# Kernel optimization log

Hardware: AMD Instinct MI355X
Metric: run time of the kernel (lower is better)

The kernel has to match this reference:

```python
import jax, jax.numpy as jnp
import numpy as np

N_HEADS = 8  # from init_kwargs; only used for the softmax scale


def setup_inputs() -> dict:
    key = jax.random.key(0)
    k1, k2, k3 = jax.random.split(key, 3)
    B, S, D = 4, 4096, 1024
    inputs = jax.random.normal(k1, (B, S, 2 * D), dtype=jnp.float32)
    W_qkv = jax.random.normal(k2, (2 * D, 3 * D), dtype=jnp.float32) * (1.0 / np.sqrt(2 * D))
    W_ff = jax.random.normal(k3, (D, D), dtype=jnp.float32) * (1.0 / np.sqrt(D))
    b_ff = jnp.zeros((D,), dtype=jnp.float32)
    return {"inputs": inputs, "W_qkv": W_qkv, "W_ff": W_ff, "b_ff": b_ff}


def reference(inputs, W_qkv, W_ff, b_ff):
    D = W_ff.shape[0]
    dim_head = D / N_HEADS
    scale = 1.0 / np.sqrt(dim_head)
    kqv = inputs @ W_qkv                       # [B, S, 3D]
    k, q, v = jnp.split(kqv, 3, axis=-1)        # chunk order in source: k, q, v
    scores = jnp.einsum('bqd,bkd->bqk', q, k) * scale   # [B, S, S]
    attn = jax.nn.softmax(scores, axis=-1)
    # dropout_p is undefined in the buggy source; treated as eval-mode identity
    out = jnp.einsum('bqk,bkd->bqd', attn, v)   # [B, S, D]
    return out @ W_ff + b_ff
```

## Files before the change

### kernel.cpp

```cpp
#include <hip/hip_runtime.h>

typedef unsigned short u16;
using bf16x8 = __attribute__((ext_vector_type(8))) __bf16;
using f32x4  = __attribute__((ext_vector_type(4))) float;
using u16x8  = __attribute__((ext_vector_type(8))) u16;

__device__ __forceinline__ u16 f2bf(float f) {
    unsigned u = __builtin_bit_cast(unsigned, f);
    u += 0x7FFFu + ((u >> 16) & 1u);
    return (u16)(u >> 16);
}
__device__ __forceinline__ float bf2f(u16 h) {
    unsigned u = ((unsigned)h) << 16;
    return __builtin_bit_cast(float, u);
}
__device__ __forceinline__ u16 to_bf(float f) { return f2bf(f); }
__device__ __forceinline__ u16 to_bf(u16 h)   { return h; }

__device__ __forceinline__ void gload_lds16(const u16* g, u16* l) {
    __builtin_amdgcn_global_load_lds(
        (const __attribute__((address_space(1))) unsigned int*)g,
        (__attribute__((address_space(3))) unsigned int*)l,
        16, 0, 0);
}

__global__ __launch_bounds__(256) void k_cvt_f32_bf16(const float* __restrict__ in,
                                                      u16* __restrict__ out, long n) {
    long i = ((long)blockIdx.x * 256 + threadIdx.x) * 8;
    if (i + 8 > n) return;
    f32x4 a = *(const f32x4*)(in + i);
    f32x4 b = *(const f32x4*)(in + i + 4);
    u16x8 o;
    o[0] = f2bf(a[0]); o[1] = f2bf(a[1]); o[2] = f2bf(a[2]); o[3] = f2bf(a[3]);
    o[4] = f2bf(b[0]); o[5] = f2bf(b[1]); o[6] = f2bf(b[2]); o[7] = f2bf(b[3]);
    *(u16x8*)(out + i) = o;
}

template <typename T>
__global__ __launch_bounds__(256) void k_transpose_bf16(
    const T* __restrict__ in, long in_rs, long in_bs,
    u16* __restrict__ out, long out_rs, long out_bs, int R, int C) {
    __shared__ u16 tile[32][33];
    const int b = blockIdx.z;
    const T* ip = in + (long)b * in_bs;
    u16* op = out + (long)b * out_bs;
    const int tx = threadIdx.x, ty = threadIdx.y;
    const long r0 = (long)blockIdx.y * 32, c0 = (long)blockIdx.x * 32;
#pragma unroll
    for (int i = 0; i < 4; ++i) {
        int r = ty + i * 8;
        tile[r][tx] = to_bf(ip[(r0 + r) * in_rs + c0 + tx]);
    }
    __syncthreads();
#pragma unroll
    for (int i = 0; i < 4; ++i) {
        int c = ty + i * 8;
        op[(c0 + c) * out_rs + r0 + tx] = tile[tx][c];
    }
}

__global__ __launch_bounds__(256) void k_rowsum_recip(const u16* __restrict__ P,
                                                      float* __restrict__ out, int C) {
    const long row = blockIdx.x;
    const u16* p = P + row * (long)C;
    float s = 0.f;
    for (int c = threadIdx.x * 8; c < C; c += 256 * 8) {
        u16x8 v = *(const u16x8*)(p + c);
#pragma unroll
        for (int j = 0; j < 8; ++j) s += bf2f(v[j]);
    }
#pragma unroll
    for (int off = 32; off > 0; off >>= 1) s += __shfl_down(s, off);
    __shared__ float wsum[4];
    const int lane = threadIdx.x & 63, wid = threadIdx.x >> 6;
    if (lane == 0) wsum[wid] = s;
    __syncthreads();
    if (threadIdx.x == 0) out[row] = 1.0f / (wsum[0] + wsum[1] + wsum[2] + wsum[3]);
}


#define LGK0 asm volatile("s_waitcnt lgkmcnt(0)" ::: "memory")
#define VM4  asm volatile("s_waitcnt vmcnt(4)" ::: "memory")
#define VM0  asm volatile("s_waitcnt vmcnt(0)" ::: "memory")
#define SCHB __builtin_amdgcn_sched_barrier(0)
#define BAR  __builtin_amdgcn_s_barrier()

template <int EPI>
__global__ __launch_bounds__(512, 2) void k_gemm8(
    const u16* __restrict__ Ag, long lda, long sA,
    const u16* __restrict__ Bg, long ldb, long sB,
    void* __restrict__ Cv, long ldc, long sC,
    int K, float scale, const float* __restrict__ rrowZ, long sR,
    const float* __restrict__ bias) {
    __shared__ __align__(16) u16 As[2][2][256 * 32];
    __shared__ __align__(16) u16 Bs[2][2][256 * 32];

    const int tid = threadIdx.x;
    const int lane = tid & 63, wid = tid >> 6;
    const int wm = wid >> 2, wn = wid & 3;
    const int z = blockIdx.z;
    const long m0 = (long)blockIdx.y * 256;
    const long n0 = (long)blockIdx.x * 256;
    const u16* A = Ag + (long)z * sA;
    const u16* B = Bg + (long)z * sB;

    int st_idx[2]; long aRow[2], bRow[2];
#pragma unroll
    for (int c = 0; c < 2; ++c) {
        int d_lin = (wid * 2 + c) * 1024 + lane * 16;
        int d_log = d_lin ^ (((d_lin >> 9) & 1) << 5);
        int r = d_log >> 6, kk = (d_log & 63) >> 1;
        st_idx[c] = (wid * 2 + c) * 512;
        aRow[c] = (m0 + r) * lda + kk;
        bRow[c] = (n0 + r) * ldb + kk;
    }
    const int aBase = (wm * 128 + (lane & 15)) * 64 + (lane >> 4) * 16;
    const int bBase = (wn * 64 + (lane & 15)) * 64 + (lane >> 4) * 16;

#define STG_A(pb, ks, kt) do { \
        gload_lds16(A + aRow[0] + (kt) + (ks) * 32, &As[pb][ks][st_idx[0]]); \
        gload_lds16(A + aRow[1] + (kt) + (ks) * 32, &As[pb][ks][st_idx[1]]); } while (0)
#define STG_B(pb, ks, kt) do { \
        gload_lds16(B + bRow[0] + (kt) + (ks) * 32, &Bs[pb][ks][st_idx[0]]); \
        gload_lds16(B + bRow[1] + (kt) + (ks) * 32, &Bs[pb][ks][st_idx[1]]); } while (0)
#define LD_A(dst, mf, ks, pb) do { int _o = aBase + (mf) * 1024; \
        _o ^= ((_o >> 9) & 1) << 5; \
        (dst) = *(const bf16x8*)((const char*)&As[pb][ks][0] + _o); } while (0)
#define LD_B(dst, nf, ks, pb) do { int _o = bBase + (nf) * 1024; \
        _o ^= ((_o >> 9) & 1) << 5; \
        (dst) = *(const bf16x8*)((const char*)&Bs[pb][ks][0] + _o); } while (0)
#define MM16(mb) do { \
        _Pragma("unroll") for (int mf = 0; mf < 4; ++mf) \
        _Pragma("unroll") for (int nf = 0; nf < 4; ++nf) \
            acc[(mb) + mf][nf] = __builtin_amdgcn_mfma_f32_16x16x32_bf16( \
                afr[mf], bfr[nf], acc[(mb) + mf][nf], 0, 0, 0); } while (0)

#define KTILE(pb, STG, ktn) do { \
         \
        _Pragma("unroll") for (int i = 0; i < 4; ++i) LD_A(afr[i], i, 0, pb); \
        _Pragma("unroll") for (int i = 0; i < 4; ++i) LD_B(bfr[i], i, 0, pb); \
        if (STG) STG_A((pb) ^ 1, 0, ktn); \
        BAR; LGK0; SCHB; \
        __builtin_amdgcn_s_setprio(1); MM16(0); __builtin_amdgcn_s_setprio(0); \
        BAR; \
         \
        _Pragma("unroll") for (int i = 0; i < 4; ++i) LD_A(afr[i], 4 + i, 0, pb); \
        if (STG) STG_B((pb) ^ 1, 0, ktn); \
        BAR; LGK0; SCHB; \
        __builtin_amdgcn_s_setprio(1); MM16(4); __builtin_amdgcn_s_setprio(0); \
        if (STG) { VM4; } else { VM0; } \
        BAR; SCHB; \
         \
        _Pragma("unroll") for (int i = 0; i < 4; ++i) LD_A(afr[i], i, 1, pb); \
        _Pragma("unroll") for (int i = 0; i < 4; ++i) LD_B(bfr[i], i, 1, pb); \
        if (STG) STG_A((pb) ^ 1, 1, ktn); \
        BAR; LGK0; SCHB; \
        __builtin_amdgcn_s_setprio(1); MM16(0); __builtin_amdgcn_s_setprio(0); \
        BAR; \
         \
        _Pragma("unroll") for (int i = 0; i < 4; ++i) LD_A(afr[i], 4 + i, 1, pb); \
        if (STG) STG_B((pb) ^ 1, 1, ktn); \
        BAR; LGK0; SCHB; \
        __builtin_amdgcn_s_setprio(1); MM16(4); __builtin_amdgcn_s_setprio(0); \
        if (STG) { VM4; } \
        BAR; SCHB; \
    } while (0)

    f32x4 acc[8][4] = {};
    bf16x8 afr[4], bfr[4];

    STG_A(0, 0, 0); STG_B(0, 0, 0); STG_A(0, 1, 0); STG_B(0, 1, 0);
    VM4;
    BAR; SCHB;

    const int NT = K >> 6;
    int p = 0;
    for (int t = 0; t < NT - 1; ++t) {
        KTILE(p, 1, (t + 1) * 64);
        p ^= 1;
    }
    KTILE(p, 0, 0);

    const int r_in = (lane >> 4) * 4;
    const int c_in = lane & 15;
    const float* rr = (EPI == 2) ? (rrowZ + (long)z * sR) : nullptr;
#pragma unroll
    for (int mf = 0; mf < 8; ++mf) {
#pragma unroll
        for (int nf = 0; nf < 4; ++nf) {
            const long cg = n0 + wn * 64 + nf * 16 + c_in;
#pragma unroll
            for (int j = 0; j < 4; ++j) {
                const long rg = m0 + wm * 128 + mf * 16 + r_in + j;
                float v = acc[mf][nf][j];
                if constexpr (EPI == 0) {
                    ((u16*)Cv)[(long)z * sC + rg * ldc + cg] = f2bf(v);
                } else if constexpr (EPI == 1) {
                    ((u16*)Cv)[(long)z * sC + rg * ldc + cg] = f2bf(__expf(v * scale));
                } else if constexpr (EPI == 2) {
                    ((u16*)Cv)[(long)z * sC + rg * ldc + cg] = f2bf(v * rr[rg]);
                } else {
                    ((float*)Cv)[(long)z * sC + rg * ldc + cg] = v + bias[cg];
                }
            }
        }
    }
#undef KTILE
#undef MM16
#undef LD_A
#undef LD_B
#undef STG_A
#undef STG_B
}

extern "C" void kernel_launch(void* const* d_in, const int* in_sizes, int n_in,
                              void* d_out, int out_size, void* d_ws, size_t ws_size,
                              hipStream_t stream) {
    (void)in_sizes; (void)n_in; (void)out_size;
    const int S = 4096;
    const long BS = 4L * S;
    const float* x_f    = (const float*)d_in[0];
    const float* Wqkv_f = (const float*)d_in[1];
    const float* Wff_f  = (const float*)d_in[2];
    const float* bff    = (const float*)d_in[3];
    float* out = (float*)d_out;

    const size_t need4 = 67108864UL + 12582912UL + 2097152UL + 100663296UL +
                         33554432UL + 4UL * 33554432UL + 33554432UL + 65536UL;
    const bool batched = ws_size >= need4;
    const int Z = batched ? 4 : 1;

    char* p = (char*)d_ws;
    u16* x_bf  = (u16*)p; p += BS * 2048 * 2;
    u16* WqkvT = (u16*)p; p += 3072L * 2048 * 2;
    u16* WffT  = (u16*)p; p += 1024L * 1024 * 2;
    u16* kqv   = (u16*)p; p += BS * 3072 * 2;
    u16* vT    = (u16*)p; p += 4L * 1024 * 4096 * 2;
    u16* probs = (u16*)p; p += (long)Z * 4096L * 4096 * 2;
    u16* attn  = (u16*)p; p += BS * 1024 * 2;
    float* rrow = (float*)p; p += (long)Z * 4096L * 4;

    k_cvt_f32_bf16<<<dim3((unsigned)(BS * 2048 / 2048)), 256, 0, stream>>>(x_f, x_bf, BS * 2048);
    k_transpose_bf16<float><<<dim3(3072 / 32, 2048 / 32, 1), dim3(32, 8), 0, stream>>>(
        Wqkv_f, 3072, 0, WqkvT, 2048, 0, 2048, 3072);
    k_transpose_bf16<float><<<dim3(1024 / 32, 1024 / 32, 1), dim3(32, 8), 0, stream>>>(
        Wff_f, 1024, 0, WffT, 1024, 0, 1024, 1024);

    k_gemm8<0><<<dim3(3072 / 256, 16384 / 256, 1), 512, 0, stream>>>(
        x_bf, 2048, 0, WqkvT, 2048, 0, kqv, 3072, 0, 2048, 0.f, nullptr, 0, nullptr);

    k_transpose_bf16<u16><<<dim3(1024 / 32, 4096 / 32, 4), dim3(32, 8), 0, stream>>>(
        kqv + 2048, 3072, (long)S * 3072, vT, 4096, 1024L * 4096, 4096, 1024);

    const float scale = 0.08838834764831845f;
    for (int b = 0; b < 4; b += Z) {
        const u16* kbase = kqv + (long)b * S * 3072;
        k_gemm8<1><<<dim3(4096 / 256, 4096 / 256, Z), 512, 0, stream>>>(
            kbase + 1024, 3072, (long)S * 3072, kbase, 3072, (long)S * 3072,
            probs, 4096, (long)S * S, 1024, scale, nullptr, 0, nullptr);
        k_rowsum_recip<<<Z * 4096, 256, 0, stream>>>(probs, rrow, 4096);
        k_gemm8<2><<<dim3(1024 / 256, 4096 / 256, Z), 512, 0, stream>>>(
            probs, 4096, (long)S * S, vT + (long)b * 1024 * 4096, 4096, 1024L * 4096,
            attn + (long)b * S * 1024, 1024, (long)S * 1024,
            4096, 0.f, rrow, 4096, nullptr);
    }

    k_gemm8<3><<<dim3(1024 / 256, 16384 / 256, 1), 512, 0, stream>>>(
        attn, 1024, 0, WffT, 1024, 0, out, 1024, 0, 1024, 0.f, nullptr, 0, bff);
}
```

Baseline: 742.0 us.

## Double-buffer MFMA register fragments to overlap LDS reads with matrix math

Replaces the single set of A/B register fragments with two ping-pong sets in the GEMM main loop. The LDS reads for the next MFMA block are issued before the current block's MFMAs, and partial lgkmcnt waits (4/8) replace full waits. The goal is to hide LDS read latency behind MFMA execution. It raises register pressure under the 512-thread, 2-block launch bound, and the hand-tuned wait counts and barriers have to stay exactly right for correctness.

After: 745.3 us. About the same (+0.4%).

```diff
diff --git a/kernel.cpp b/kernel.cpp
--- a/kernel.cpp
+++ b/kernel.cpp
@@ -79,11 +79,12 @@
 }
 
 
-#define LGK0 asm volatile("s_waitcnt lgkmcnt(0)" ::: "memory")
-#define VM4  asm volatile("s_waitcnt vmcnt(4)" ::: "memory")
-#define VM0  asm volatile("s_waitcnt vmcnt(0)" ::: "memory")
-#define SCHB __builtin_amdgcn_sched_barrier(0)
-#define BAR  __builtin_amdgcn_s_barrier()
+#define LGK(n) asm volatile("s_waitcnt lgkmcnt(" #n ")" ::: "memory")
+#define VMC(n) asm volatile("s_waitcnt vmcnt(" #n ")" ::: "memory")
+#define SCHB   __builtin_amdgcn_sched_barrier(0)
+#define BAR    __builtin_amdgcn_s_barrier()
+#define PRIO1  __builtin_amdgcn_s_setprio(1)
+#define PRIO0  __builtin_amdgcn_s_setprio(0)
 
 template <int EPI>
 __global__ __launch_bounds__(512, 2) void k_gemm8(
@@ -123,63 +124,79 @@
 #define STG_B(pb, ks, kt) do { \
         gload_lds16(B + bRow[0] + (kt) + (ks) * 32, &Bs[pb][ks][st_idx[0]]); \
         gload_lds16(B + bRow[1] + (kt) + (ks) * 32, &Bs[pb][ks][st_idx[1]]); } while (0)
-#define LD_A(dst, mf, ks, pb) do { int _o = aBase + (mf) * 1024; \
-        _o ^= ((_o >> 9) & 1) << 5; \
-        (dst) = *(const bf16x8*)((const char*)&As[pb][ks][0] + _o); } while (0)
-#define LD_B(dst, nf, ks, pb) do { int _o = bBase + (nf) * 1024; \
-        _o ^= ((_o >> 9) & 1) << 5; \
-        (dst) = *(const bf16x8*)((const char*)&Bs[pb][ks][0] + _o); } while (0)
-#define MM16(mb) do { \
+#define LD4_A(dst, h, ks, pb) do { \
+        _Pragma("unroll") for (int _i = 0; _i < 4; ++_i) { \
+            int _o = aBase + ((h) * 4 + _i) * 1024; \
+            _o ^= ((_o >> 9) & 1) << 5; \
+            dst[_i] = *(const bf16x8*)((const char*)&As[pb][ks][0] + _o); } } while (0)
+#define LD4_B(dst, ks, pb) do { \
+        _Pragma("unroll") for (int _i = 0; _i < 4; ++_i) { \
+            int _o = bBase + _i * 1024; \
+            _o ^= ((_o >> 9) & 1) << 5; \
+            dst[_i] = *(const bf16x8*)((const char*)&Bs[pb][ks][0] + _o); } } while (0)
+#define MM16(mb, af, bf) do { \
         _Pragma("unroll") for (int mf = 0; mf < 4; ++mf) \
         _Pragma("unroll") for (int nf = 0; nf < 4; ++nf) \
             acc[(mb) + mf][nf] = __builtin_amdgcn_mfma_f32_16x16x32_bf16( \
-                afr[mf], bfr[nf], acc[(mb) + mf][nf], 0, 0, 0); } while (0)
-
-#define KTILE(pb, STG, ktn) do { \
-         \
-        _Pragma("unroll") for (int i = 0; i < 4; ++i) LD_A(afr[i], i, 0, pb); \
-        _Pragma("unroll") for (int i = 0; i < 4; ++i) LD_B(bfr[i], i, 0, pb); \
-        if (STG) STG_A((pb) ^ 1, 0, ktn); \
-        BAR; LGK0; SCHB; \
-        __builtin_amdgcn_s_setprio(1); MM16(0); __builtin_amdgcn_s_setprio(0); \
-        BAR; \
-         \
-        _Pragma("unroll") for (int i = 0; i < 4; ++i) LD_A(afr[i], 4 + i, 0, pb); \
-        if (STG) STG_B((pb) ^ 1, 0, ktn); \
-        BAR; LGK0; SCHB; \
-        __builtin_amdgcn_s_setprio(1); MM16(4); __builtin_amdgcn_s_setprio(0); \
-        if (STG) { VM4; } else { VM0; } \
-        BAR; SCHB; \
-         \
-        _Pragma("unroll") for (int i = 0; i < 4; ++i) LD_A(afr[i], i, 1, pb); \
-        _Pragma("unroll") for (int i = 0; i < 4; ++i) LD_B(bfr[i], i, 1, pb); \
-        if (STG) STG_A((pb) ^ 1, 1, ktn); \
-        BAR; LGK0; SCHB; \
-        __builtin_amdgcn_s_setprio(1); MM16(0); __builtin_amdgcn_s_setprio(0); \
-        BAR; \
-         \
-        _Pragma("unroll") for (int i = 0; i < 4; ++i) LD_A(afr[i], 4 + i, 1, pb); \
-        if (STG) STG_B((pb) ^ 1, 1, ktn); \
-        BAR; LGK0; SCHB; \
-        __builtin_amdgcn_s_setprio(1); MM16(4); __builtin_amdgcn_s_setprio(0); \
-        if (STG) { VM4; } \
-        BAR; SCHB; \
-    } while (0)
+                af[mf], bf[nf], acc[(mb) + mf][nf], 0, 0, 0); } while (0)
 
     f32x4 acc[8][4] = {};
-    bf16x8 afr[4], bfr[4];
+    bf16x8 afrA[4], afrB[4], bfrA[4], bfrB[4];
 
     STG_A(0, 0, 0); STG_B(0, 0, 0); STG_A(0, 1, 0); STG_B(0, 1, 0);
-    VM4;
+    VMC(4);
     BAR; SCHB;
+    LD4_A(afrA, 0, 0, 0);
+    LD4_B(bfrA, 0, 0);
 
     const int NT = K >> 6;
-    int p = 0;
     for (int t = 0; t < NT - 1; ++t) {
-        KTILE(p, 1, (t + 1) * 64);
-        p ^= 1;
-    }
-    KTILE(p, 0, 0);
+        const int p = t & 1;
+        const long ktn = (long)(t + 1) * 64;
+        LD4_A(afrB, 1, 0, p);
+        STG_A(p ^ 1, 0, ktn);
+        BAR; LGK(4); SCHB;
+        PRIO1; MM16(0, afrA, bfrA); PRIO0;
+        VMC(2); SCHB;
+        BAR;
+        LD4_A(afrA, 0, 1, p);
+        LD4_B(bfrB, 1, p);
+        STG_B(p ^ 1, 0, ktn);
+        BAR; LGK(8); SCHB;
+        PRIO1; MM16(4, afrB, bfrA); PRIO0;
+        BAR;
+        LD4_A(afrB, 1, 1, p);
+        STG_A(p ^ 1, 1, ktn);
+        BAR; LGK(4); SCHB;
+        PRIO1; MM16(0, afrA, bfrB); PRIO0;
+        VMC(2); SCHB;
+        BAR;
+        LD4_A(afrA, 0, 0, p ^ 1);
+        LD4_B(bfrA, 0, p ^ 1);
+        STG_B(p ^ 1, 1, ktn);
+        BAR; LGK(8); SCHB;
+        PRIO1; MM16(4, afrB, bfrB); PRIO0;
+        BAR;
+    }
+    {
+        const int p = (NT - 1) & 1;
+        LD4_A(afrB, 1, 0, p);
+        BAR; LGK(4); SCHB;
+        PRIO1; MM16(0, afrA, bfrA); PRIO0;
+        VMC(0); SCHB;
+        BAR;
+        LD4_A(afrA, 0, 1, p);
+        LD4_B(bfrB, 1, p);
+        BAR; LGK(8); SCHB;
+        PRIO1; MM16(4, afrB, bfrA); PRIO0;
+        BAR;
+        LD4_A(afrB, 1, 1, p);
+        BAR; LGK(4); SCHB;
+        PRIO1; MM16(0, afrA, bfrB); PRIO0;
+        BAR;
+        LGK(0); SCHB;
+        PRIO1; MM16(4, afrB, bfrB); PRIO0;
+    }
 
     const int r_in = (lane >> 4) * 4;
     const int c_in = lane & 15;
@@ -205,10 +222,9 @@
             }
         }
     }
-#undef KTILE
 #undef MM16
-#undef LD_A
-#undef LD_B
+#undef LD4_A
+#undef LD4_B
 #undef STG_A
 #undef STG_B
 }
```
